# Optimization experiments

Measured on AMD Instinct MI355X. Metric: run time of the kernel, lower is better.

## Reference

```python
import jax, jax.numpy as jnp
import numpy as np

D_MODEL = 768
N_HEAD = 12
D_HEAD = 64


def setup_inputs() -> dict:
    key = jax.random.key(0)
    k1, k2, k3, k4, k5 = jax.random.split(key, 5)
    B, T = 8, 1024
    hidden_states = jax.random.normal(k1, (B, T, D_MODEL), dtype=jnp.float32)
    # torch Linear weights are [out, in]; we store [in, out] and use x @ W
    scale_attn = 1.0 / np.sqrt(D_MODEL)
    W_attn = jax.random.normal(k2, (D_MODEL, 3 * D_MODEL), dtype=jnp.float32) * scale_attn
    b_attn = jax.random.normal(k3, (3 * D_MODEL,), dtype=jnp.float32) * 0.02
    W_proj = jax.random.normal(k4, (D_MODEL, D_MODEL), dtype=jnp.float32) * scale_attn
    b_proj = jax.random.normal(k5, (D_MODEL,), dtype=jnp.float32) * 0.02
    return {"hidden_states": hidden_states, "W_attn": W_attn, "b_attn": b_attn,
            "W_proj": W_proj, "b_proj": b_proj}


def reference(hidden_states, W_attn, b_attn, W_proj, b_proj):
    B, T, _ = hidden_states.shape
    qkv = hidden_states @ W_attn + b_attn                     # [B, T, 3*D]
    Q, K, V = jnp.split(qkv, 3, axis=-1)
    def heads(x):  # [B, T, D] -> [B, H, T, d]
        return x.reshape(B, T, N_HEAD, D_HEAD).transpose(0, 2, 1, 3)
    Q, K, V = heads(Q), heads(K), heads(V)
    # past_key_values=None -> T_full == T, q_start == 0: standard causal mask
    scores = jnp.einsum('bhqd,bhkd->bhqk', Q, K) / np.sqrt(D_HEAD)
    causal = jnp.tril(jnp.ones((T, T), dtype=bool))
    scores = jnp.where(causal, scores, -jnp.inf)
    attn = jax.nn.softmax(scores, axis=-1)
    values = jnp.einsum('bhqk,bhkd->bhqd', attn, V)          # dropout = identity (eval)
    values = values.transpose(0, 2, 1, 3).reshape(B, T, D_MODEL)
    out = values @ W_proj + b_proj
    return out, K, V
```

## Files before the change

### kernel.cpp

```cpp
#include <hip/hip_runtime.h>
#include <stdint.h>

#define B_SZ 8
#define T_SZ 1024
#define DM   768
#define NH   12
#define DH   64
#define NTOK (B_SZ * T_SZ)
#define NOUT (NTOK * DM)
#define INF  __builtin_inff()

typedef unsigned short u16;
typedef __attribute__((ext_vector_type(8))) short short8;
typedef __attribute__((ext_vector_type(4))) short short4v;
typedef __attribute__((ext_vector_type(4))) float f32x4;

#define MFMA16x16x32 __builtin_amdgcn_mfma_f32_16x16x32_bf16

__device__ __forceinline__ u16 f2bf(float f) {
    unsigned u = __builtin_bit_cast(unsigned, f);
    u += 0x7fffu + ((u >> 16) & 1u);
    return (u16)(u >> 16);
}

__device__ __forceinline__ f32x4 max4(f32x4 a, f32x4 b) {
    f32x4 r; r.x = fmaxf(a.x, b.x); r.y = fmaxf(a.y, b.y);
    r.z = fmaxf(a.z, b.z); r.w = fmaxf(a.w, b.w); return r;
}
__device__ __forceinline__ f32x4 add4(f32x4 a, f32x4 b) {
    f32x4 r; r.x = a.x + b.x; r.y = a.y + b.y;
    r.z = a.z + b.z; r.w = a.w + b.w; return r;
}

__device__ __forceinline__ void gload16(const void* g, void* l) {
    __builtin_amdgcn_global_load_lds(
        (const __attribute__((address_space(1))) unsigned int*)(unsigned long long)(uintptr_t)g,
        (__attribute__((address_space(3))) unsigned int*)(unsigned int)(uintptr_t)l,
        16, 0, 0);
}

__global__ __launch_bounds__(256) void cvt_bf16_kernel(const float* __restrict__ in,
                                                       u16* __restrict__ out, int n) {
    int i = (blockIdx.x * 256 + threadIdx.x) * 4;
    if (i >= n) return;
    f32x4 v = *(const f32x4*)(in + i);
    short4v o;
    o.x = (short)f2bf(v.x); o.y = (short)f2bf(v.y);
    o.z = (short)f2bf(v.z); o.w = (short)f2bf(v.w);
    *(short4v*)(out + i) = o;
}

__global__ __launch_bounds__(256) void transpose_bf16_kernel(const float* __restrict__ in,
                                                             u16* __restrict__ out,
                                                             int R, int C) {
    __shared__ float tile[32][33];
    int tx = threadIdx.x & 31, ty = threadIdx.x >> 5;
    int c0 = blockIdx.x * 32, r0 = blockIdx.y * 32;
    for (int i = ty; i < 32; i += 8)
        tile[i][tx] = in[(size_t)(r0 + i) * C + c0 + tx];
    __syncthreads();
    for (int i = ty; i < 32; i += 8)
        out[(size_t)(c0 + i) * R + r0 + tx] = f2bf(tile[tx][i]);
}

__global__ __launch_bounds__(256) void transpose_v_kernel(const float* __restrict__ in,
                                                          u16* __restrict__ out) {
    __shared__ float tile[32][33];
    const int head = blockIdx.z;
    const int t0 = blockIdx.x * 32, d0 = blockIdx.y * 32;
    const float* ip = in + (size_t)head * 65536;
    u16* op = out + (size_t)head * 65536;
    int tx = threadIdx.x & 31, ty = threadIdx.x >> 5;
    for (int i = ty; i < 32; i += 8)
        tile[i][tx] = ip[(size_t)(t0 + i) * 64 + d0 + tx];
    __syncthreads();
    for (int i = ty; i < 32; i += 8)
        op[(size_t)(d0 + i) * 1024 + t0 + tx] = f2bf(tile[tx][i]);
}

template <int EPI>
__global__ __launch_bounds__(256, 4) void gemm_k768_kernel(
    const u16* __restrict__ A, const u16* __restrict__ BT, const float* __restrict__ bias,
    u16* __restrict__ qbf, u16* __restrict__ kbf,
    float* __restrict__ outK, float* __restrict__ outV, float* __restrict__ outP)
{
    __shared__ alignas(16) u16 As[2][128 * 32];
    __shared__ alignas(16) u16 Bs[2][128 * 32];
    const int t   = threadIdx.x;
    const int wid = t >> 6, l = t & 63;
    const int lr  = l & 15, g = l >> 4;
    const int m0  = blockIdx.x * 128, n0 = blockIdx.y * 128;
    const int wm  = (wid >> 1) * 64, wn = (wid & 1) * 64;

    const int srow = t >> 2;
    const int sch  = (t & 3) ^ (srow & 3);
    const u16* ga0 = A  + (size_t)(m0 + srow) * 768 + sch * 8;
    const u16* ga1 = A  + (size_t)(m0 + 64 + srow) * 768 + sch * 8;
    const u16* gb0 = BT + (size_t)(n0 + srow) * 768 + sch * 8;
    const u16* gb1 = BT + (size_t)(n0 + 64 + srow) * 768 + sch * 8;

#define GSTAGE(buf, k0) do {                              \
        gload16(ga0 + (k0), As[buf] + t * 8);             \
        gload16(ga1 + (k0), As[buf] + 2048 + t * 8);      \
        gload16(gb0 + (k0), Bs[buf] + t * 8);             \
        gload16(gb1 + (k0), Bs[buf] + 2048 + t * 8);      \
    } while (0)

    const int fco = (g ^ (lr & 3)) * 8;

    f32x4 acc[4][4] = {};
    GSTAGE(0, 0);
    __syncthreads();
    int cur = 0;
    #pragma unroll 1
    for (int k0 = 32; k0 <= 768; k0 += 32) {
        if (k0 < 768) GSTAGE(cur ^ 1, k0);
        const u16* aB = As[cur];
        const u16* bB = Bs[cur];
        short8 af[4], bfr[4];
        #pragma unroll
        for (int i = 0; i < 4; ++i)
            af[i] = *(const short8*)(aB + (wm + i * 16 + lr) * 32 + fco);
        #pragma unroll
        for (int j = 0; j < 4; ++j)
            bfr[j] = *(const short8*)(bB + (wn + j * 16 + lr) * 32 + fco);
        __builtin_amdgcn_s_setprio(1);
        #pragma unroll
        for (int i = 0; i < 4; ++i)
            #pragma unroll
            for (int j = 0; j < 4; ++j)
                acc[i][j] = MFMA16x16x32(af[i], bfr[j], acc[i][j], 0, 0, 0);
        __builtin_amdgcn_s_setprio(0);
        __syncthreads();
        cur ^= 1;
    }
#undef GSTAGE

    #pragma unroll
    for (int j = 0; j < 4; ++j) {
        const int n = n0 + wn + j * 16 + lr;
        const float bn = bias[n];
        if (EPI == 0) {
            const int which = n / 768;
            const int hd = n - which * 768;
            const int h = hd >> 6, dd = hd & 63;
            #pragma unroll
            for (int i = 0; i < 4; ++i) {
                #pragma unroll
                for (int r = 0; r < 4; ++r) {
                    const int m = m0 + wm + i * 16 + g * 4 + r;
                    const int b = m >> 10, tt = m & 1023;
                    const int idx = ((b * 12 + h) * 1024 + tt) * 64 + dd;
                    const float v = acc[i][j][r] + bn;
                    if (which == 0) {
                        qbf[idx] = f2bf(v * (0.125f * 1.44269504f));
                    } else if (which == 1) {
                        outK[idx] = v; kbf[idx] = f2bf(v);
                    } else {
                        outV[idx] = v;
                    }
                }
            }
        } else {
            #pragma unroll
            for (int i = 0; i < 4; ++i)
                #pragma unroll
                for (int r = 0; r < 4; ++r) {
                    const int m = m0 + wm + i * 16 + g * 4 + r;
                    outP[(size_t)m * 768 + n] = acc[i][j][r] + bn;
                }
        }
    }
}

__global__ __launch_bounds__(256, 3) void attn_kernel(
    const u16* __restrict__ Qb, const u16* __restrict__ Kb,
    const u16* __restrict__ Vt, u16* __restrict__ Ob)
{
    __shared__ alignas(16) u16 Ks[2][4096];
    __shared__ alignas(16) u16 Vs[2][4096];
    __shared__ alignas(16) u16 Pl[4][16 * 72];
    const int bh = blockIdx.x;
    const int t = threadIdx.x;
    const int wid = t >> 6, l = t & 63;
    const int c = l & 15, g = l >> 4;
    u16* P = Pl[wid];
    const u16* Kp = Kb + (size_t)bh * 65536;
    const u16* Vp = Vt + (size_t)bh * 65536;
    const int b = bh / 12, h = bh - (bh / 12) * 12;

    const int srow = t >> 3;
    const int sch  = (t & 7) ^ (srow & 7);
    const u16* Ksrc0 = Kp + (size_t)srow * 64 + sch * 8;
    const u16* Ksrc1 = Kp + (size_t)(srow + 32) * 64 + sch * 8;
    const u16* Vsrc0 = Vp + (size_t)srow * 1024 + sch * 8;
    const u16* Vsrc1 = Vp + (size_t)(srow + 32) * 1024 + sch * 8;

    const int fo0 = c * 64 + ((g ^ (c & 7)) * 8);
    const int fo1 = c * 64 + (((g + 4) ^ (c & 7)) * 8);

#define STAGE(buf, kt0) do {                                        \
        gload16(Ksrc0 + (size_t)(kt0) * 64, Ks[buf] + t * 8);       \
        gload16(Ksrc1 + (size_t)(kt0) * 64, Ks[buf] + 2048 + t * 8);\
        gload16(Vsrc0 + (kt0),              Vs[buf] + t * 8);       \
        gload16(Vsrc1 + (kt0),              Vs[buf] + 2048 + t * 8);\
    } while (0)

    #pragma unroll 1
    for (int pass = 0; pass < 2; ++pass) {
        const int tile = pass ? (15 - blockIdx.y) : blockIdx.y;
        const int qbase = tile * 64 + wid * 16;
        const int qg = qbase + c;
        const u16* Qp = Qb + ((size_t)bh * 1024 + qg) * 64 + g * 8;
        const short8 bq0 = *(const short8*)(Qp);
        const short8 bq1 = *(const short8*)(Qp + 32);

        f32x4 oacc[4] = {};
        float mrow = -INF, lpart = 0.f;
        const int nb = tile + 1;

        STAGE(0, 0);
        __syncthreads();
        int cur = 0;

        #pragma unroll 1
        for (int kb = 0; kb < nb; ++kb) {
            if (kb + 1 < nb) STAGE(cur ^ 1, (kb + 1) << 6);
            const u16* kB = Ks[cur];
            const u16* vB = Vs[cur];
            short8 af0[4], af1[4], vf0[4], vf1[4];
            #pragma unroll
            for (int j = 0; j < 4; ++j) {
                af0[j] = *(const short8*)(kB + j * 1024 + fo0);
                af1[j] = *(const short8*)(kB + j * 1024 + fo1);
            }
            #pragma unroll
            for (int dt = 0; dt < 4; ++dt) {
                vf0[dt] = *(const short8*)(vB + dt * 1024 + fo0);
                vf1[dt] = *(const short8*)(vB + dt * 1024 + fo1);
            }
            f32x4 s[4] = {};
            __builtin_amdgcn_s_setprio(1);
            #pragma unroll
            for (int j = 0; j < 4; ++j) {
                s[j] = MFMA16x16x32(af0[j], bq0, s[j], 0, 0, 0);
                s[j] = MFMA16x16x32(af1[j], bq1, s[j], 0, 0, 0);
            }
            __builtin_amdgcn_s_setprio(0);
            if (kb == nb - 1) {
                const int kt0 = kb << 6;
                #pragma unroll
                for (int j = 0; j < 4; ++j)
                    #pragma unroll
                    for (int r = 0; r < 4; ++r)
                        if (kt0 + j * 16 + g * 4 + r > qg) s[j][r] = -INF;
            }
            f32x4 mm = max4(max4(s[0], s[1]), max4(s[2], s[3]));
            float tm = fmaxf(fmaxf(mm.x, mm.y), fmaxf(mm.z, mm.w));
            tm = fmaxf(tm, __shfl_xor(tm, 16));
            tm = fmaxf(tm, __shfl_xor(tm, 32));
            const bool keep = (__all(tm <= mrow + 8.f) != 0);
            const float mnew = keep ? mrow : fmaxf(mrow, tm);
            if (!keep) {
                const float sc = exp2f(mrow - mnew);
                mrow = mnew;
                lpart *= sc;
                #pragma unroll
                for (int dt = 0; dt < 4; ++dt) {
                    oacc[dt][0] *= sc; oacc[dt][1] *= sc;
                    oacc[dt][2] *= sc; oacc[dt][3] *= sc;
                }
            }
            f32x4 p[4];
            #pragma unroll
            for (int j = 0; j < 4; ++j) {
                p[j].x = exp2f(s[j].x - mnew); p[j].y = exp2f(s[j].y - mnew);
                p[j].z = exp2f(s[j].z - mnew); p[j].w = exp2f(s[j].w - mnew);
            }
            f32x4 ps = add4(add4(p[0], p[1]), add4(p[2], p[3]));
            lpart += (ps.x + ps.y) + (ps.z + ps.w);
            #pragma unroll
            for (int j = 0; j < 4; ++j) {
                short4v w;
                w.x = (short)f2bf(p[j].x); w.y = (short)f2bf(p[j].y);
                w.z = (short)f2bf(p[j].z); w.w = (short)f2bf(p[j].w);
                *(short4v*)(P + c * 72 + j * 16 + g * 4) = w;
            }
            const short8 pf0 = *(const short8*)(P + c * 72 + g * 8);
            const short8 pf1 = *(const short8*)(P + c * 72 + 32 + g * 8);
            __builtin_amdgcn_s_setprio(1);
            #pragma unroll
            for (int dt = 0; dt < 4; ++dt) {
                oacc[dt] = MFMA16x16x32(vf0[dt], pf0, oacc[dt], 0, 0, 0);
                oacc[dt] = MFMA16x16x32(vf1[dt], pf1, oacc[dt], 0, 0, 0);
            }
            __builtin_amdgcn_s_setprio(0);
            __syncthreads();
            cur ^= 1;
        }
        float lsum = lpart;
        lsum += __shfl_xor(lsum, 16);
        lsum += __shfl_xor(lsum, 32);
        const float li = 1.f / lsum;
        #pragma unroll
        for (int dt = 0; dt < 4; ++dt) {
            short4v o;
            o.x = (short)f2bf(oacc[dt][0] * li);
            o.y = (short)f2bf(oacc[dt][1] * li);
            o.z = (short)f2bf(oacc[dt][2] * li);
            o.w = (short)f2bf(oacc[dt][3] * li);
            *(short4v*)(Ob + (size_t)(b * 1024 + qg) * 768 + h * 64 + dt * 16 + g * 4) = o;
        }
    }
#undef STAGE
}

extern "C" void kernel_launch(void* const* d_in, const int* in_sizes, int n_in,
                              void* d_out, int out_size, void* d_ws, size_t ws_size,
                              hipStream_t stream) {
    const float* hs = (const float*)d_in[0];
    const float* Wa = (const float*)d_in[1];
    const float* ba = (const float*)d_in[2];
    const float* Wp = (const float*)d_in[3];
    const float* bp = (const float*)d_in[4];
    float* out = (float*)d_out;

    u16* ws  = (u16*)d_ws;
    u16* Xbf = ws;
    u16* WaT = Xbf + NOUT;
    u16* WpT = WaT + 768 * 2304;
    u16* Qbf = WpT + 768 * 768;
    u16* Kbf = Qbf + NOUT;
    u16* VTb = Kbf + NOUT;
    u16* Obf = VTb + NOUT;

    cvt_bf16_kernel<<<NOUT / 1024, 256, 0, stream>>>(hs, Xbf, NOUT);
    transpose_bf16_kernel<<<dim3(2304 / 32, 768 / 32), 256, 0, stream>>>(Wa, WaT, 768, 2304);
    transpose_bf16_kernel<<<dim3(768 / 32, 768 / 32), 256, 0, stream>>>(Wp, WpT, 768, 768);
    gemm_k768_kernel<0><<<dim3(64, 18), 256, 0, stream>>>(
        Xbf, WaT, ba, Qbf, Kbf, out + NOUT, out + 2 * (size_t)NOUT, nullptr);
    transpose_v_kernel<<<dim3(32, 2, 96), 256, 0, stream>>>(out + 2 * (size_t)NOUT, VTb);
    attn_kernel<<<dim3(96, 8), 256, 0, stream>>>(Qbf, Kbf, VTb, Obf);
    gemm_k768_kernel<1><<<dim3(64, 6), 256, 0, stream>>>(
        Obf, WpT, bp, nullptr, nullptr, nullptr, nullptr, out);
}
```

Baseline: 133.4 us.

## Deepen GEMM pipeline to four LDS stages with explicit vmcnt waits

The K=768 GEMM moves from double buffering to a four-buffer ring that prefetches three k-tiles ahead. The full __syncthreads is replaced by explicit s_waitcnt vmcnt counts plus s_barrier, so later loads can stay in flight across iterations. The LDS swizzle is also changed to XOR on (row>>1)&3 to alter the bank-conflict pattern. LDS use doubles, so launch bounds drop from 4 to 2 blocks per CU, which risks lower occupancy.

New measurement: 130.6 us. 1.02x faster.

```diff
diff --git a/kernel.cpp b/kernel.cpp
--- a/kernel.cpp
+++ b/kernel.cpp
@@ -79,13 +79,13 @@
 }
 
 template <int EPI>
-__global__ __launch_bounds__(256, 4) void gemm_k768_kernel(
+__global__ __launch_bounds__(256, 2) void gemm_k768_kernel(
     const u16* __restrict__ A, const u16* __restrict__ BT, const float* __restrict__ bias,
     u16* __restrict__ qbf, u16* __restrict__ kbf,
     float* __restrict__ outK, float* __restrict__ outV, float* __restrict__ outP)
 {
-    __shared__ alignas(16) u16 As[2][128 * 32];
-    __shared__ alignas(16) u16 Bs[2][128 * 32];
+    __shared__ alignas(16) u16 As[4][128 * 32];
+    __shared__ alignas(16) u16 Bs[4][128 * 32];
     const int t   = threadIdx.x;
     const int wid = t >> 6, l = t & 63;
     const int lr  = l & 15, g = l >> 4;
@@ -93,30 +93,33 @@
     const int wm  = (wid >> 1) * 64, wn = (wid & 1) * 64;
 
     const int srow = t >> 2;
-    const int sch  = (t & 3) ^ (srow & 3);
-    const u16* ga0 = A  + (size_t)(m0 + srow) * 768 + sch * 8;
-    const u16* ga1 = A  + (size_t)(m0 + 64 + srow) * 768 + sch * 8;
-    const u16* gb0 = BT + (size_t)(n0 + srow) * 768 + sch * 8;
-    const u16* gb1 = BT + (size_t)(n0 + 64 + srow) * 768 + sch * 8;
-
-#define GSTAGE(buf, k0) do {                              \
-        gload16(ga0 + (k0), As[buf] + t * 8);             \
-        gload16(ga1 + (k0), As[buf] + 2048 + t * 8);      \
-        gload16(gb0 + (k0), Bs[buf] + t * 8);             \
-        gload16(gb1 + (k0), Bs[buf] + 2048 + t * 8);      \
+    const int sch  = ((t & 3) ^ ((srow >> 1) & 3)) * 8;
+    const u16* ga0 = A  + (size_t)(m0 + srow) * 768 + sch;
+    const u16* ga1 = A  + (size_t)(m0 + 64 + srow) * 768 + sch;
+    const u16* gb0 = BT + (size_t)(n0 + srow) * 768 + sch;
+    const u16* gb1 = BT + (size_t)(n0 + 64 + srow) * 768 + sch;
+
+#define GSTAGE(buf, kt) do {                              \
+        gload16(ga0 + (kt) * 32, As[buf] + t * 8);        \
+        gload16(ga1 + (kt) * 32, As[buf] + 2048 + t * 8); \
+        gload16(gb0 + (kt) * 32, Bs[buf] + t * 8);        \
+        gload16(gb1 + (kt) * 32, Bs[buf] + 2048 + t * 8); \
     } while (0)
 
-    const int fco = (g ^ (lr & 3)) * 8;
+    const int fco = (g ^ ((lr >> 1) & 3)) * 8;
 
     f32x4 acc[4][4] = {};
-    GSTAGE(0, 0);
-    __syncthreads();
-    int cur = 0;
+    GSTAGE(0, 0); GSTAGE(1, 1); GSTAGE(2, 2);
+    asm volatile("s_waitcnt vmcnt(8)" ::: "memory");
+    __builtin_amdgcn_s_barrier();
+    __builtin_amdgcn_sched_barrier(0);
+
     #pragma unroll 1
-    for (int k0 = 32; k0 <= 768; k0 += 32) {
-        if (k0 < 768) GSTAGE(cur ^ 1, k0);
-        const u16* aB = As[cur];
-        const u16* bB = Bs[cur];
+    for (int kt = 0; kt < 24; ++kt) {
+        const int buf = kt & 3;
+        if (kt < 21) GSTAGE((kt + 3) & 3, kt + 3);
+        const u16* aB = As[buf];
+        const u16* bB = Bs[buf];
         short8 af[4], bfr[4];
         #pragma unroll
         for (int i = 0; i < 4; ++i)
@@ -131,8 +134,11 @@
             for (int j = 0; j < 4; ++j)
                 acc[i][j] = MFMA16x16x32(af[i], bfr[j], acc[i][j], 0, 0, 0);
         __builtin_amdgcn_s_setprio(0);
-        __syncthreads();
-        cur ^= 1;
+        if (kt < 21)       asm volatile("s_waitcnt vmcnt(8)" ::: "memory");
+        else if (kt == 21) asm volatile("s_waitcnt vmcnt(4)" ::: "memory");
+        else if (kt == 22) asm volatile("s_waitcnt vmcnt(0)" ::: "memory");
+        __builtin_amdgcn_s_barrier();
+        __builtin_amdgcn_sched_barrier(0);
     }
 #undef GSTAGE
 
```
